# Performance work log

Hardware: AMD Instinct MI355X
Metric: run time of the kernel (lower is better)

The kernel has to match this reference:

```python
import jax, jax.numpy as jnp
import numpy as np

PI_2 = 3.14159 / 2  # matches the torch module's pi_2 constant
EPS = 1e-8          # F.cosine_similarity default eps


def setup_inputs() -> dict:
    key = jax.random.key(0)
    k1, k2 = jax.random.split(key)
    B, N, C, H, W = 32, 2000, 512, 7, 7
    key_t = jax.random.normal(k1, (B, C, H, W), dtype=jnp.float32)
    memory = jax.random.normal(k2, (N, C, H, W), dtype=jnp.float32)
    return {"key": key_t, "memory": memory}


def reference(key, memory):
    # Memory.read(key): cosine-similarity addressing + tan warp + softmax, then weighted read.
    B = key.shape[0]
    N = memory.shape[0]
    k = key.reshape(B, -1)        # [B, D], D = C*H*W
    m = memory.reshape(N, -1)     # [N, D]
    # cosine similarity with torch's eps clamping on norms
    dots = jnp.einsum('bd,nd->bn', k, m)                                   # [B, N]
    k_norm = jnp.maximum(jnp.sqrt(jnp.sum(k * k, axis=-1, keepdims=True)), EPS)  # [B, 1]
    m_norm = jnp.maximum(jnp.sqrt(jnp.sum(m * m, axis=-1)), EPS)                 # [N]
    cos = dots / (k_norm * m_norm[None, :])                                 # [B, N]
    w = jax.nn.softmax(jnp.tan(cos * PI_2), axis=1)                         # [B, N]
    # weighted read: sum_n w[b,n] * memory[n,c,h,w] -> [B, C, H, W]
    out = jnp.einsum('bn,nchw->bchw', w, memory)
    return out
```

## Files before the change

### kernel.cpp

```cpp
#include <hip/hip_runtime.h>
#include <math.h>

#define D_ELEMS 25088
#define D4      6272
#define N_MEM   2000
#define B_KEYS  32
#define PI_2F   1.570795f
#define EPSF    1e-8f
#define NSLICE  49
#define KSLICE  512
#define KSTEPS  16
#define NTILE   250

using short8 = __attribute__((ext_vector_type(8))) short;
using short4v = __attribute__((ext_vector_type(4))) short;
using f32x4  = __attribute__((ext_vector_type(4))) float;


__device__ inline short f2bf(float x) {
    union { float f; unsigned u; } v; v.f = x;
    unsigned r = v.u + 0x7fffu + ((v.u >> 16) & 1u);
    return (short)(r >> 16);
}

__global__ __launch_bounds__(256) void k_prep(const float* __restrict__ key,
                                              short* __restrict__ keyb,
                                              float* __restrict__ knorm) {
    const int b   = blockIdx.x;
    const int tid = threadIdx.x;
    const float4* K4 = (const float4*)(key + (size_t)b * D_ELEMS);
    short4v* KB4 = (short4v*)keyb + (size_t)b * D4;
    float ks = 0.f;
    for (int i = tid; i < D4; i += 256) {
        const float4 f = K4[i];
        short4v s;
        s[0] = f2bf(f.x); s[1] = f2bf(f.y); s[2] = f2bf(f.z); s[3] = f2bf(f.w);
        KB4[i] = s;
        ks += f.x * f.x + f.y * f.y + f.z * f.z + f.w * f.w;
    }
#pragma unroll
    for (int o = 1; o < 64; o <<= 1) ks += __shfl_xor(ks, o, 64);
    __shared__ float sred[4];
    if ((tid & 63) == 0) sred[tid >> 6] = ks;
    __syncthreads();
    if (tid == 0)
        knorm[b] = fmaxf(sqrtf(sred[0] + sred[1] + sred[2] + sred[3]), EPSF);
}

__global__ __launch_bounds__(64) void k_dots_mfma(const short* __restrict__ keyb,
                                                  const float* __restrict__ mem,
                                                  float* __restrict__ dots_part,
                                                  float* __restrict__ mn2_part) {
    const int nt   = blockIdx.x / NSLICE;
    const int s    = blockIdx.x % NSLICE;
    const int n0   = nt * 16;
    const int lane = threadIdx.x;
    const int quad = lane >> 4;
    const int l16  = lane & 15;
    const int k0   = s * KSLICE + quad * 8;

    const short* a0p = keyb + (size_t)l16 * D_ELEMS + k0;
    const short* a1p = keyb + (size_t)(16 + l16) * D_ELEMS + k0;
    const float4* bp = (const float4*)(mem + (size_t)(n0 + l16) * D_ELEMS + k0);

    f32x4 acc0 = {0.f, 0.f, 0.f, 0.f};
    f32x4 acc1 = {0.f, 0.f, 0.f, 0.f};
    float msq = 0.f;

    short8 a0 = *(const short8*)a0p;
    short8 a1 = *(const short8*)a1p;
    float4 f0 = bp[0], f1 = bp[1];

    for (int t = 0; t < KSTEPS; ++t) {
        const short8 a0c = a0, a1c = a1;
        const float4 f0c = f0, f1c = f1;
        if (t + 1 < KSTEPS) {
            a0 = *(const short8*)(a0p + (t + 1) * 32);
            a1 = *(const short8*)(a1p + (t + 1) * 32);
            f0 = bp[(t + 1) * 8];
            f1 = bp[(t + 1) * 8 + 1];
        }
        msq += f0c.x * f0c.x + f0c.y * f0c.y + f0c.z * f0c.z + f0c.w * f0c.w
             + f1c.x * f1c.x + f1c.y * f1c.y + f1c.z * f1c.z + f1c.w * f1c.w;
        short8 b;
        b[0] = f2bf(f0c.x); b[1] = f2bf(f0c.y); b[2] = f2bf(f0c.z); b[3] = f2bf(f0c.w);
        b[4] = f2bf(f1c.x); b[5] = f2bf(f1c.y); b[6] = f2bf(f1c.z); b[7] = f2bf(f1c.w);
        acc0 = __builtin_amdgcn_mfma_f32_16x16x32_bf16(a0c, b, acc0, 0, 0, 0);
        acc1 = __builtin_amdgcn_mfma_f32_16x16x32_bf16(a1c, b, acc1, 0, 0, 0);
    }

    float* dp = dots_part + (size_t)(s * N_MEM + n0 + l16) * B_KEYS;
#pragma unroll
    for (int r = 0; r < 4; ++r) {
        dp[quad * 4 + r]      = acc0[r];
        dp[16 + quad * 4 + r] = acc1[r];
    }

    msq += __shfl_xor(msq, 16, 64);
    msq += __shfl_xor(msq, 32, 64);
    if (lane < 16) mn2_part[s * N_MEM + n0 + lane] = msq;
}

__global__ __launch_bounds__(256) void k_reduce(const float* __restrict__ dots_part,
                                                const float* __restrict__ mn2_part,
                                                float* __restrict__ dots,
                                                float* __restrict__ mn2) {
    const int gid = blockIdx.x * 256 + threadIdx.x;
    float ds = 0.f;
#pragma unroll
    for (int s = 0; s < NSLICE; ++s) ds += dots_part[s * (N_MEM * B_KEYS) + gid];
    dots[gid] = ds;
    if (gid < N_MEM) {
        float ms = 0.f;
#pragma unroll
        for (int s = 0; s < NSLICE; ++s) ms += mn2_part[s * N_MEM + gid];
        mn2[gid] = ms;
    }
}

__global__ __launch_bounds__(512) void k_softmax(const float* __restrict__ knormArr,
                                                 const float* __restrict__ dots,
                                                 const float* __restrict__ mn2,
                                                 float* __restrict__ w) {
    const int b   = blockIdx.x;
    const int tid = threadIdx.x;
    __shared__ float sred[512];
    __shared__ float xbuf[N_MEM];
    const float knorm = knormArr[b];

    float mx = -1e30f;
    for (int n = tid; n < N_MEM; n += 512) {
        const float mn = fmaxf(sqrtf(mn2[n]), EPSF);
        const float x  = __tanf((dots[n * B_KEYS + b] / (knorm * mn)) * PI_2F);
        xbuf[n] = x;
        mx = fmaxf(mx, x);
    }
    sred[tid] = mx;
    __syncthreads();
    for (int o = 256; o; o >>= 1) {
        if (tid < o) sred[tid] = fmaxf(sred[tid], sred[tid + o]);
        __syncthreads();
    }
    mx = sred[0];
    __syncthreads();

    float sm = 0.f;
    for (int n = tid; n < N_MEM; n += 512) {
        const float e = __expf(xbuf[n] - mx);
        xbuf[n] = e;
        sm += e;
    }
    sred[tid] = sm;
    __syncthreads();
    for (int o = 256; o; o >>= 1) {
        if (tid < o) sred[tid] += sred[tid + o];
        __syncthreads();
    }
    const float inv = 1.f / sred[0];

    for (int n = tid; n < N_MEM; n += 512)
        w[n * B_KEYS + b] = xbuf[n] * inv;
}

__global__ __launch_bounds__(256, 4) void k_read(const float* __restrict__ mem,
                                                 const float* __restrict__ w,
                                                 float* __restrict__ partial,
                                                 int nPerS) {
    const int db   = blockIdx.x % 98;
    const int s    = blockIdx.x / 98;
    const int n0   = s * nPerS;
    const int bg   = threadIdx.x >> 6;
    const int lane = threadIdx.x & 63;
    const int d4   = db * 64 + lane;

    const float4* M4 = (const float4*)mem;
    const float4* W4 = (const float4*)w;
    __shared__ float4 wls4[NTILE * 8];

    float acc[8][4];
#pragma unroll
    for (int i = 0; i < 8; ++i)
#pragma unroll
        for (int j = 0; j < 4; ++j) acc[i][j] = 0.f;

    for (int c0 = 0; c0 < nPerS; c0 += NTILE) {
        __syncthreads();
        for (int i = threadIdx.x; i < NTILE * 8; i += 256)
            wls4[i] = W4[(size_t)(n0 + c0) * 8 + i];
        __syncthreads();

        const float4* mp = M4 + (size_t)(n0 + c0) * D4 + d4;
#pragma unroll 5
        for (int nn = 0; nn < NTILE; ++nn) {
            const float4 mc = mp[(size_t)nn * D4];
            const float4 wa = wls4[nn * 8 + bg * 2];
            const float4 wb = wls4[nn * 8 + bg * 2 + 1];
            const float wv[8] = {wa.x, wa.y, wa.z, wa.w, wb.x, wb.y, wb.z, wb.w};
#pragma unroll
            for (int i = 0; i < 8; ++i) {
                acc[i][0] += wv[i] * mc.x;
                acc[i][1] += wv[i] * mc.y;
                acc[i][2] += wv[i] * mc.z;
                acc[i][3] += wv[i] * mc.w;
            }
        }
    }

    float4* P4 = (float4*)partial;
#pragma unroll
    for (int i = 0; i < 8; ++i)
        P4[(size_t)(s * B_KEYS + bg * 8 + i) * D4 + d4] =
            make_float4(acc[i][0], acc[i][1], acc[i][2], acc[i][3]);
}

__global__ __launch_bounds__(256) void k_finish(const float* __restrict__ partial,
                                                float* __restrict__ out, int ns) {
    const int i = blockIdx.x * 256 + threadIdx.x;
    const float4* P4 = (const float4*)partial;
    float4 sum = P4[i];
    for (int s = 1; s < ns; ++s) {
        const float4 p = P4[(size_t)s * (B_KEYS * D4) + i];
        sum.x += p.x; sum.y += p.y; sum.z += p.z; sum.w += p.w;
    }
    ((float4*)out)[i] = sum;
}

extern "C" void kernel_launch(void* const* d_in, const int* in_sizes, int n_in,
                              void* d_out, int out_size, void* d_ws, size_t ws_size,
                              hipStream_t stream) {
    (void)in_sizes; (void)n_in; (void)out_size;
    const float* key = (const float*)d_in[0];
    const float* mem = (const float*)d_in[1];
    float* out = (float*)d_out;
    float* ws  = (float*)d_ws;

    short* keyb      = (short*)ws;
    float* dots_part = ws + 401408;
    float* mn2_part  = ws + 3537408;
    float* dots      = ws + 3635408;
    float* mn2       = ws + 3699408;
    float* knorm     = ws + 3701408;
    float* w         = ws + 3701440;
    float* part      = ws + 3765440;

    int ns = 8;
    while (ns > 1 && (size_t)(3765440 + (size_t)ns * 802816) * 4 > ws_size) ns >>= 1;
    const int nPerS = N_MEM / ns;

    k_prep     <<<B_KEYS, 256, 0, stream>>>(key, keyb, knorm);
    k_dots_mfma<<<125 * NSLICE, 64, 0, stream>>>(keyb, mem, dots_part, mn2_part);
    k_reduce   <<<250, 256, 0, stream>>>(dots_part, mn2_part, dots, mn2);
    k_softmax  <<<B_KEYS, 512, 0, stream>>>(knorm, dots, mn2, w);
    k_read     <<<98 * ns, 256, 0, stream>>>(mem, w, part, nPerS);
    k_finish   <<<784, 256, 0, stream>>>(part, out, ns);
}
```

Before: 375.5 us.

## Restructure read kernel to 32 keys per thread and widen prep/dots launches

```diff
diff --git a/kernel.cpp b/kernel.cpp
--- a/kernel.cpp
+++ b/kernel.cpp
@@ -10,7 +10,8 @@
 #define NSLICE  49
 #define KSLICE  512
 #define KSTEPS  16
-#define NTILE   250
+#define NWAVES  (125 * NSLICE)
+#define RTILE   100
 
 using short8 = __attribute__((ext_vector_type(8))) short;
 using short4v = __attribute__((ext_vector_type(4))) short;
@@ -24,37 +25,23 @@
 }
 
 __global__ __launch_bounds__(256) void k_prep(const float* __restrict__ key,
-                                              short* __restrict__ keyb,
-                                              float* __restrict__ knorm) {
-    const int b   = blockIdx.x;
-    const int tid = threadIdx.x;
-    const float4* K4 = (const float4*)(key + (size_t)b * D_ELEMS);
-    short4v* KB4 = (short4v*)keyb + (size_t)b * D4;
-    float ks = 0.f;
-    for (int i = tid; i < D4; i += 256) {
-        const float4 f = K4[i];
-        short4v s;
-        s[0] = f2bf(f.x); s[1] = f2bf(f.y); s[2] = f2bf(f.z); s[3] = f2bf(f.w);
-        KB4[i] = s;
-        ks += f.x * f.x + f.y * f.y + f.z * f.z + f.w * f.w;
-    }
-#pragma unroll
-    for (int o = 1; o < 64; o <<= 1) ks += __shfl_xor(ks, o, 64);
-    __shared__ float sred[4];
-    if ((tid & 63) == 0) sred[tid >> 6] = ks;
-    __syncthreads();
-    if (tid == 0)
-        knorm[b] = fmaxf(sqrtf(sred[0] + sred[1] + sred[2] + sred[3]), EPSF);
-}
-
-__global__ __launch_bounds__(64) void k_dots_mfma(const short* __restrict__ keyb,
+                                              short* __restrict__ keyb) {
+    const int i = blockIdx.x * 256 + threadIdx.x;
+    const float4 f = ((const float4*)key)[i];
+    short4v s; s[0] = f2bf(f.x); s[1] = f2bf(f.y); s[2] = f2bf(f.z); s[3] = f2bf(f.w);
+    ((short4v*)keyb)[i] = s;
+}
+
+__global__ __launch_bounds__(256) void k_dots_mfma(const short* __restrict__ keyb,
                                                   const float* __restrict__ mem,
                                                   float* __restrict__ dots_part,
                                                   float* __restrict__ mn2_part) {
-    const int nt   = blockIdx.x / NSLICE;
-    const int s    = blockIdx.x % NSLICE;
+    const int wid = blockIdx.x * 4 + (threadIdx.x >> 6);
+    if (wid >= NWAVES) return;
+    const int nt   = wid / NSLICE;
+    const int s    = wid % NSLICE;
     const int n0   = nt * 16;
-    const int lane = threadIdx.x;
+    const int lane = threadIdx.x & 63;
     const int quad = lane >> 4;
     const int l16  = lane & 15;
     const int k0   = s * KSLICE + quad * 8;
@@ -118,7 +105,7 @@
     }
 }
 
-__global__ __launch_bounds__(512) void k_softmax(const float* __restrict__ knormArr,
+__global__ __launch_bounds__(512) void k_softmax(const float* __restrict__ key,
                                                  const float* __restrict__ dots,
                                                  const float* __restrict__ mn2,
                                                  float* __restrict__ w) {
@@ -126,7 +113,21 @@
     const int tid = threadIdx.x;
     __shared__ float sred[512];
     __shared__ float xbuf[N_MEM];
-    const float knorm = knormArr[b];
+
+    const float4* K4 = (const float4*)(key + (size_t)b * D_ELEMS);
+    float ks = 0.f;
+    for (int i = tid; i < D4; i += 512) {
+        const float4 kf = K4[i];
+        ks += kf.x * kf.x + kf.y * kf.y + kf.z * kf.z + kf.w * kf.w;
+    }
+    sred[tid] = ks;
+    __syncthreads();
+    for (int o = 256; o; o >>= 1) {
+        if (tid < o) sred[tid] += sred[tid + o];
+        __syncthreads();
+    }
+    const float knorm = fmaxf(sqrtf(sred[0]), EPSF);
+    __syncthreads();
 
     float mx = -1e30f;
     for (int n = tid; n < N_MEM; n += 512) {
@@ -162,55 +163,57 @@
         w[n * B_KEYS + b] = xbuf[n] * inv;
 }
 
-__global__ __launch_bounds__(256, 4) void k_read(const float* __restrict__ mem,
+__global__ __launch_bounds__(128, 2) void k_read(const float* __restrict__ mem,
                                                  const float* __restrict__ w,
                                                  float* __restrict__ partial,
                                                  int nPerS) {
-    const int db   = blockIdx.x % 98;
-    const int s    = blockIdx.x / 98;
-    const int n0   = s * nPerS;
-    const int bg   = threadIdx.x >> 6;
-    const int lane = threadIdx.x & 63;
-    const int d4   = db * 64 + lane;
+    const int db  = blockIdx.x % 49;
+    const int s   = blockIdx.x / 49;
+    const int n0  = s * nPerS;
+    const int tid = threadIdx.x;
+    const int d4  = db * 128 + tid;
 
     const float4* M4 = (const float4*)mem;
     const float4* W4 = (const float4*)w;
-    __shared__ float4 wls4[NTILE * 8];
-
-    float acc[8][4];
-#pragma unroll
-    for (int i = 0; i < 8; ++i)
-#pragma unroll
-        for (int j = 0; j < 4; ++j) acc[i][j] = 0.f;
-
-    for (int c0 = 0; c0 < nPerS; c0 += NTILE) {
-        __syncthreads();
-        for (int i = threadIdx.x; i < NTILE * 8; i += 256)
-            wls4[i] = W4[(size_t)(n0 + c0) * 8 + i];
+    __shared__ float4 wls[RTILE * 8];
+
+    float acc[32][4];
+#pragma unroll
+    for (int i = 0; i < 32; ++i) {
+        acc[i][0] = 0.f; acc[i][1] = 0.f; acc[i][2] = 0.f; acc[i][3] = 0.f;
+    }
+
+    for (int c0 = 0; c0 < nPerS; c0 += RTILE) {
+        __syncthreads();
+        for (int i = tid; i < RTILE * 8; i += 128)
+            wls[i] = W4[(size_t)(n0 + c0) * 8 + i];
         __syncthreads();
 
         const float4* mp = M4 + (size_t)(n0 + c0) * D4 + d4;
-#pragma unroll 5
-        for (int nn = 0; nn < NTILE; ++nn) {
+#pragma unroll 4
+        for (int nn = 0; nn < RTILE; ++nn) {
             const float4 mc = mp[(size_t)nn * D4];
-            const float4 wa = wls4[nn * 8 + bg * 2];
-            const float4 wb = wls4[nn * 8 + bg * 2 + 1];
-            const float wv[8] = {wa.x, wa.y, wa.z, wa.w, wb.x, wb.y, wb.z, wb.w};
-#pragma unroll
-            for (int i = 0; i < 8; ++i) {
-                acc[i][0] += wv[i] * mc.x;
-                acc[i][1] += wv[i] * mc.y;
-                acc[i][2] += wv[i] * mc.z;
-                acc[i][3] += wv[i] * mc.w;
+#pragma unroll
+            for (int q = 0; q < 8; ++q) {
+                const float4 wq = wls[nn * 8 + q];
+                const int b0 = q * 4;
+                acc[b0+0][0] += wq.x * mc.x; acc[b0+0][1] += wq.x * mc.y;
+                acc[b0+0][2] += wq.x * mc.z; acc[b0+0][3] += wq.x * mc.w;
+                acc[b0+1][0] += wq.y * mc.x; acc[b0+1][1] += wq.y * mc.y;
+                acc[b0+1][2] += wq.y * mc.z; acc[b0+1][3] += wq.y * mc.w;
+                acc[b0+2][0] += wq.z * mc.x; acc[b0+2][1] += wq.z * mc.y;
+                acc[b0+2][2] += wq.z * mc.z; acc[b0+2][3] += wq.z * mc.w;
+                acc[b0+3][0] += wq.w * mc.x; acc[b0+3][1] += wq.w * mc.y;
+                acc[b0+3][2] += wq.w * mc.z; acc[b0+3][3] += wq.w * mc.w;
             }
         }
     }
 
     float4* P4 = (float4*)partial;
 #pragma unroll
-    for (int i = 0; i < 8; ++i)
-        P4[(size_t)(s * B_KEYS + bg * 8 + i) * D4 + d4] =
-            make_float4(acc[i][0], acc[i][1], acc[i][2], acc[i][3]);
+    for (int b = 0; b < 32; ++b)
+        P4[(size_t)(s * B_KEYS + b) * D4 + d4] =
+            make_float4(acc[b][0], acc[b][1], acc[b][2], acc[b][3]);
 }
 
 __global__ __launch_bounds__(256) void k_finish(const float* __restrict__ partial,
@@ -239,18 +242,18 @@
     float* mn2_part  = ws + 3537408;
     float* dots      = ws + 3635408;
     float* mn2       = ws + 3699408;
-    float* knorm     = ws + 3701408;
     float* w         = ws + 3701440;
     float* part      = ws + 3765440;
 
-    int ns = 8;
-    while (ns > 1 && (size_t)(3765440 + (size_t)ns * 802816) * 4 > ws_size) ns >>= 1;
+    int ns = 20;
+    while (ns > 1 && (size_t)(3765440 + (size_t)ns * 802816) * 4 > ws_size)
+        ns = (ns == 20) ? 10 : (ns == 10) ? 5 : (ns == 5) ? 2 : 1;
     const int nPerS = N_MEM / ns;
 
-    k_prep     <<<B_KEYS, 256, 0, stream>>>(key, keyb, knorm);
-    k_dots_mfma<<<125 * NSLICE, 64, 0, stream>>>(keyb, mem, dots_part, mn2_part);
+    k_prep     <<<784, 256, 0, stream>>>(key, keyb);
+    k_dots_mfma<<<(NWAVES + 3) / 4, 256, 0, stream>>>(keyb, mem, dots_part, mn2_part);
     k_reduce   <<<250, 256, 0, stream>>>(dots_part, mn2_part, dots, mn2);
-    k_softmax  <<<B_KEYS, 512, 0, stream>>>(knorm, dots, mn2, w);
-    k_read     <<<98 * ns, 256, 0, stream>>>(mem, w, part, nPerS);
+    k_softmax  <<<B_KEYS, 512, 0, stream>>>(key, dots, mn2, w);
+    k_read     <<<49 * ns, 128, 0, stream>>>(mem, w, part, nPerS);
     k_finish   <<<784, 256, 0, stream>>>(part, out, ns);
 }
```

Result: slower. 392.1 us (+4.4%).
